# Optimization experiments

Hardware: AMD Instinct MI355X
Metric: run time of the kernel (lower is better)

## Reference

```python
import jax, jax.numpy as jnp
import numpy as np

GL16 = [5, 3, 3, 3, 3, 3, 5, 5, 5, 11, 3, 3, 3, 3, 3, 12]  # sum 73
GL7 = [5, 9, 9, 25, 9, 9, 12]  # sum 78
BN_EPS = 1e-5
LRELU_SLOPE = 0.01


def setup_inputs() -> dict:
    key = jax.random.key(0)
    ks = jax.random.split(key, 32)
    B = 65536
    u = lambda k, shp, s: jax.random.uniform(k, shp, minval=-s, maxval=s)
    inp = {}
    inp['x'] = jax.random.normal(ks[0], (B, 310), dtype=jnp.float32)
    # learned adjacency (convert_dis_m(get_ini_dis_m(), 9) placeholder)
    inp['adj'] = jax.random.normal(ks[1], (62, 62), dtype=jnp.float32) * 0.1
    s5 = 1.0 / np.sqrt(5.0)
    inp['lgcn_w'] = u(ks[2], (5, 5), s5)
    inp['lgcn_b'] = u(ks[3], (5,), s5)
    # ChannelAttentionMPL (frequency, C=5) conv1d k=1 weights [out,in]
    inp['ca1_w1'] = jax.random.normal(ks[4], (32, 5)) * 0.3
    inp['ca1_w2'] = jax.random.normal(ks[5], (5, 32)) * 0.1
    # ChannelAttentionMPL (channel, C=62)
    inp['ca2_w1'] = jax.random.normal(ks[6], (32, 62)) * 0.1
    inp['ca2_w2'] = jax.random.normal(ks[7], (62, 32)) * 0.1
    # MesoLayer weights [5,10]
    inp['meso1_w'] = u(ks[8], (5, 10), 1.0 / np.sqrt(78.0))
    inp['meso2_w'] = u(ks[9], (5, 10), 1.0 / np.sqrt(78.0))
    # graphpool.feature_trans index maps (channel gathers into 62 channels)
    inp['idx16'] = jax.random.randint(ks[10], (73,), 0, 62, dtype=jnp.int32)
    inp['idx7'] = jax.random.randint(ks[11], (78,), 0, 62, dtype=jnp.int32)
    # MLP head 735->256->128->64 with eval-mode BatchNorm params
    def lin(ka, kb, fin, fout):
        s = 1.0 / np.sqrt(fin)
        return u(ka, (fin, fout), s), u(kb, (fout,), s)
    inp['w1'], inp['b1'] = lin(ks[12], ks[13], 735, 256)
    inp['w2'], inp['b2'] = lin(ks[14], ks[15], 256, 128)
    inp['w3'], inp['b3'] = lin(ks[16], ks[17], 128, 64)
    for i, (nm, d) in enumerate([('1', 256), ('2', 128), ('3', 64)]):
        inp['g' + nm] = 1.0 + 0.1 * jax.random.normal(ks[18 + 3 * i], (d,))
        inp['be' + nm] = 0.1 * jax.random.normal(ks[19 + 3 * i], (d,))
        inp['m' + nm] = 0.05 * jax.random.normal(ks[20 + 3 * i], (d,))
        inp['v' + nm] = jnp.ones((d,), dtype=jnp.float32)
    return inp


def channel_attention(x, w1, w2):
    # x: [B, C, L]; SE-style attention with avg+max pooling over L
    avg = jnp.mean(x, axis=2)            # [B, C]
    mx = jnp.max(x, axis=2)              # [B, C]
    def mlp(z):
        return jax.nn.relu(z @ w1.T) @ w2.T   # [B, C]
    att = jax.nn.sigmoid(mlp(avg) + mlp(mx))[:, :, None]  # [B, C, 1]
    return x + att * x, att


def meso(feat, idx, weight, graph_list):
    # feat: [B, 62, 5]; gather channels then per-subgraph attention pooling
    f = feat[:, idx]                     # [B, L, 5]
    outs = []
    h = 0
    for n in graph_list:                 # fixed small structural loop
        sub = jax.lax.dynamic_slice_in_dim(f, h, n, axis=1)  # [B, n, 5]
        fw = jnp.einsum('bjg,gh->bjh', sub, weight)          # [B, n, 10]
        # sum_i (fw @ fw^T)[b,j,i] == fw[b,j,:] . sum_i fw[b,i,:]
        scores = jnp.einsum('bjh,bh->bj', fw, jnp.sum(fw, axis=1))  # [B, n]
        att = jax.nn.softmax(scores, axis=1)
        outs.append(jnp.einsum('bj,bjg->bg', att, sub))      # [B, 5]
        h += n
    return jnp.stack(outs, axis=1)       # [B, S, 5]


def _forward(x, adj, lgcn_w, lgcn_b, ca1_w1, ca1_w2, ca2_w1, ca2_w2,
             meso1_w, meso2_w, idx16, idx7,
             w1, b1, g1, be1, m1, v1,
             w2, b2, g2, be2, m2, v2,
             w3, b3, g3, be3, m3, v3):
    B = x.shape[0]
    h = x.reshape(B, 5, 62).transpose(0, 2, 1)                   # [B, 62, 5]
    wf = jnp.einsum('bij,jd->bid', h, lgcn_w)
    h = jnp.einsum('ij,bjd->bid', adj, wf) + lgcn_b              # LocalLayer
    residual = h
    hx = h.transpose(0, 2, 1)                                    # [B, 5, 62]
    x_flat = hx.reshape(B, -1)                                   # [B, 310]
    out, att1 = channel_attention(hx, ca1_w1, ca1_w2)            # [B, 5, 62]
    out, att2 = channel_attention(out.transpose(0, 2, 1), ca2_w1, ca2_w2)  # [B,62,5]
    x1 = meso(residual, idx16, meso1_w, GL16).transpose(0, 2, 1).reshape(B, -1)  # [B, 80]
    x3 = meso(residual, idx7, meso2_w, GL7).transpose(0, 2, 1).reshape(B, -1)    # [B, 35]
    out_flat = out.transpose(0, 2, 1).reshape(B, -1)             # [B, 310]
    cat = jnp.concatenate([x_flat, out_flat, x1, x3], axis=1)    # [B, 735]

    def block(z, w, b, g, be, m, v):
        y = z @ w + b
        y = (y - m) / jnp.sqrt(v + BN_EPS) * g + be              # eval BN
        return jnp.where(y > 0, y, LRELU_SLOPE * y)              # LeakyReLU

    y = block(cat, w1, b1, g1, be1, m1, v1)
    y = block(y, w2, b2, g2, be2, m2, v2)
    y = block(y, w3, b3, g3, be3, m3, v3)
    return y, att1, att2


def reference(x, adj, lgcn_w, lgcn_b, ca1_w1, ca1_w2, ca2_w1, ca2_w2,
              meso1_w, meso2_w, idx16, idx7,
              w1, b1, w2, b2, w3, b3,
              g1, be1, m1, v1, g2, be2, m2, v2, g3, be3, m3, v3):
    return _forward(x, adj, lgcn_w, lgcn_b, ca1_w1, ca1_w2, ca2_w1, ca2_w2,
                    meso1_w, meso2_w, idx16, idx7,
                    w1, b1, g1, be1, m1, v1,
                    w2, b2, g2, be2, m2, v2,
                    w3, b3, g3, be3, m3, v3)
```

## Files before the change

### kernel.cpp

```cpp
#include <hip/hip_runtime.h>
#include <math.h>

#define BN_EPS 1e-5f
#define SLOPE 0.01f

typedef _Float16 f16;
typedef _Float16 f16x8 __attribute__((ext_vector_type(8)));
typedef float f32x4 __attribute__((ext_vector_type(4)));

__device__ __constant__ int c_g16_st[16] = {0,5,8,11,14,17,20,25,30,35,46,49,52,55,58,61};
__device__ __constant__ int c_g16_n[16]  = {5,3,3,3,3,3,5,5,5,11,3,3,3,3,3,12};
__device__ __constant__ int c_g7_st[7]   = {0,5,14,23,48,57,66};
__device__ __constant__ int c_g7_n[7]    = {5,9,9,25,9,9,12};

__device__ __forceinline__ float lrelu(float y) { return y > 0.f ? y : SLOPE * y; }

template<int T, int G, int BASE>
__device__ void meso_part(const int* __restrict__ st_arr, const int* __restrict__ n_arr,
                          int lane, long b, const float* h, const int* __restrict__ idxa,
                          const float* mw, float* fwbuf, float* scbuf,
                          f16* __restrict__ catb)
{
  const int team = lane / T, slot = lane - team * T;
  int st = 0, n = 0;
  if (team < G) { st = st_arr[team]; n = n_arr[team]; }
  float sp[10] = {0,0,0,0,0,0,0,0,0,0};
  if (team < G) {
    for (int j = slot; j < n; j += T) {
      int ri = idxa[st + j];
      float sv[5];
      #pragma unroll
      for (int g = 0; g < 5; ++g) sv[g] = h[ri*8 + g];
      #pragma unroll
      for (int t = 0; t < 10; ++t) {
        float f = sv[0]*mw[t] + sv[1]*mw[10+t] + sv[2]*mw[20+t] + sv[3]*mw[30+t] + sv[4]*mw[40+t];
        fwbuf[(st+j)*10 + t] = f;
        sp[t] += f;
      }
    }
  }
  #pragma unroll
  for (int off = 1; off < T; off <<= 1) {
    #pragma unroll
    for (int t = 0; t < 10; ++t) sp[t] += __shfl_xor(sp[t], off);
  }
  __syncthreads();
  if (team < G) {
    for (int j = slot; j < n; j += T) {
      float sc = 0.f;
      #pragma unroll
      for (int t = 0; t < 10; ++t) sc += fwbuf[(st+j)*10 + t] * sp[t];
      scbuf[st + j] = sc;
    }
  }
  __syncthreads();
  float po[5] = {0,0,0,0,0};
  if (team < G) {
    float mx = -1e30f;
    for (int jj = 0; jj < n; ++jj) mx = fmaxf(mx, scbuf[st + jj]);
    float sum = 0.f;
    for (int jj = 0; jj < n; ++jj) sum += expf(scbuf[st + jj] - mx);
    float inv = 1.f / sum;
    for (int j = slot; j < n; j += T) {
      float a = expf(scbuf[st + j] - mx) * inv;
      int ri = idxa[st + j];
      #pragma unroll
      for (int g = 0; g < 5; ++g) po[g] += a * h[ri*8 + g];
    }
  }
  #pragma unroll
  for (int off = 1; off < T; off <<= 1) {
    #pragma unroll
    for (int g = 0; g < 5; ++g) po[g] += __shfl_xor(po[g], off);
  }
  if (team < G && slot == 0) {
    #pragma unroll
    for (int g = 0; g < 5; ++g) catb[b*736 + BASE + g*G + team] = (f16)po[g];
  }
}

__global__ void wcvt_kernel(const float* __restrict__ w1, const float* __restrict__ w2,
                            const float* __restrict__ w3,
                            const float* __restrict__ adj, const float* __restrict__ lgcn_w,
                            f16* __restrict__ w1T, f16* __restrict__ w2T, f16* __restrict__ w3T,
                            f16* __restrict__ Mp)
{
  int i = blockIdx.x * 256 + threadIdx.x;
  if (i < 256*736) {
    int n = i / 736, k = i - n*736;
    w1T[i] = (f16)(k < 735 ? w1[k*256 + n] : 0.f);
    return;
  }
  int j = i - 256*736;
  if (j < 128*256) {
    int n = j >> 8, k = j & 255;
    w2T[j] = (f16)w2[k*128 + n];
    return;
  }
  int q = j - 128*256;
  if (q < 64*128) {
    int n = q >> 7, k = q & 127;
    w3T[q] = (f16)w3[k*64 + n];
    return;
  }
  int m = q - 64*128;
  if (m < 320*320) {
    int col = m / 320, k = m - col*320;
    float v = 0.f;
    if (col < 310 && k < 310) {
      int d = col / 62, ii = col - d*62;
      int g = k / 62,  jj = k - g*62;
      v = adj[ii*62 + jj] * lgcn_w[g*5 + d];
    }
    Mp[m] = (f16)v;
  }
}

__global__ __launch_bounds__(256) void gemm_h(
    const float* __restrict__ x, const f16* __restrict__ Mp,
    const float* __restrict__ lgcn_b, f16* __restrict__ catb)
{
  __shared__ __align__(16) f16 a_lds[64*320];

  const int tid = threadIdx.x;
  const int wv = tid >> 6;
  const int lane = tid & 63;
  const int ln = lane & 15;
  const int kg = lane >> 4;
  const long b0 = (long)blockIdx.x * 64;

  const f16* mp[5];
  #pragma unroll
  for (int nc = 0; nc < 5; ++nc)
    mp[nc] = Mp + (size_t)(wv*80 + nc*16 + ln)*320 + kg*8;
  f16x8 bF[5], bN[5];
  #pragma unroll
  for (int nc = 0; nc < 5; ++nc) bF[nc] = *(const f16x8*)(mp[nc]);

  for (int rr = 0; rr < 16; ++rr) {
    int row = wv*16 + rr;
    if (lane < 8) {
      int c = 38 + (lane >> 2);
      *(unsigned*)((char*)a_lds + row*640 + ((c ^ (row & 7)) << 4) + (lane & 3)*4) = 0u;
    }
    const float* xr = x + (b0 + row)*310;
    for (int f = lane; f < 155; f += 64) {
      float2 v = *(const float2*)(xr + 2*f);
      int k = 2*f;
      int c = k >> 3;
      f16 h0 = (f16)v.x, h1 = (f16)v.y;
      unsigned u = (unsigned)*(unsigned short*)&h0 | ((unsigned)*(unsigned short*)&h1 << 16);
      *(unsigned*)((char*)a_lds + row*640 + ((c ^ (row & 7)) << 4) + (k & 7)*2) = u;
    }
  }
  __syncthreads();

  f32x4 zero = {0.f, 0.f, 0.f, 0.f};
  f32x4 acc[4][5];
  #pragma unroll
  for (int mr = 0; mr < 4; ++mr)
    #pragma unroll
    for (int nc = 0; nc < 5; ++nc) acc[mr][nc] = zero;

  for (int s = 0; s < 10; ++s) {
    if (s < 9) {
      #pragma unroll
      for (int nc = 0; nc < 5; ++nc) bN[nc] = *(const f16x8*)(mp[nc] + (s + 1)*32);
    }
    #pragma unroll
    for (int mr = 0; mr < 4; ++mr) {
      int r = mr*16 + ln;
      int c = s*4 + kg;
      f16x8 af = *(const f16x8*)((const char*)a_lds + r*640 + ((c ^ (r & 7)) << 4));
      #pragma unroll
      for (int nc = 0; nc < 5; ++nc)
        acc[mr][nc] = __builtin_amdgcn_mfma_f32_16x16x32_f16(af, bF[nc], acc[mr][nc], 0, 0, 0);
    }
    #pragma unroll
    for (int nc = 0; nc < 5; ++nc) bF[nc] = bN[nc];
  }

  __syncthreads();
  #pragma unroll
  for (int nc = 0; nc < 5; ++nc) {
    int n = wv*80 + nc*16 + ln;
    float bias = (n < 310) ? lgcn_b[n / 62] : 0.f;
    int c = n >> 3;
    #pragma unroll
    for (int mr = 0; mr < 4; ++mr) {
      #pragma unroll
      for (int ri = 0; ri < 4; ++ri) {
        int r = mr*16 + kg*4 + ri;
        f16 val = (f16)(acc[mr][nc][ri] + bias);
        *(f16*)((char*)a_lds + r*640 + ((c ^ (r & 7)) << 4) + (n & 7)*2) = val;
      }
    }
  }
  __syncthreads();
  for (int rr = 0; rr < 16; ++rr) {
    int row = wv*16 + rr;
    if (lane < 39) {
      int c = lane;
      f16x8 v = *(const f16x8*)((const char*)a_lds + row*640 + ((c ^ (row & 7)) << 4));
      *(f16x8*)(catb + (b0 + row)*736 + c*8) = v;
    }
  }
}

__global__ __launch_bounds__(256) void front2(
    const float* __restrict__ ca1_w1, const float* __restrict__ ca1_w2,
    const float* __restrict__ ca2_w1, const float* __restrict__ ca2_w2,
    const float* __restrict__ meso1_w, const float* __restrict__ meso2_w,
    const int* __restrict__ idx16, const int* __restrict__ idx7,
    f16* __restrict__ catb, float* __restrict__ outp, int B)
{
  __shared__ __align__(16) float h_s[4][496];
  __shared__ __align__(16) float fw_s[4][800];
  __shared__ float sc_s[4][80];
  __shared__ float t_s[4][64];
  __shared__ float small_s[4][16];
  __shared__ float v62_s[4][192];
  __shared__ float mw_s[100];

  const int tid = threadIdx.x;
  const int w = tid >> 6;
  const int lane = tid & 63;
  const long b = (long)blockIdx.x * 4 + w;

  if (tid < 50) mw_s[tid] = meso1_w[tid];
  else if (tid < 100) mw_s[tid] = meso2_w[tid - 50];

  for (int p = lane; p < 310; p += 64) {
    float v = (float)catb[b*736 + p];
    int d = p / 62, i = p - d*62;
    h_s[w][i*8 + d] = v;
  }
  __syncthreads();

  {
    int d = lane >> 3, q = lane & 7;
    float s = 0.f, m = -1e30f;
    if (d < 5) {
      #pragma unroll
      for (int e = 0; e < 8; ++e) {
        int i = q*8 + e;
        if (i < 62) { float v = h_s[w][i*8 + d]; s += v; m = fmaxf(m, v); }
      }
    }
    #pragma unroll
    for (int off = 1; off < 8; off <<= 1) {
      s += __shfl_xor(s, off);
      m = fmaxf(m, __shfl_xor(m, off));
    }
    if (d < 5 && q == 0) {
      small_s[w][d] = s * (1.f/62.f);
      small_s[w][5 + d] = m;
    }
  }
  __syncthreads();
  if (lane < 32) {
    float ta = 0.f, tm = 0.f;
    #pragma unroll
    for (int d = 0; d < 5; ++d) {
      float wv = ca1_w1[lane*5 + d];
      ta += small_s[w][d] * wv;
      tm += small_s[w][5 + d] * wv;
    }
    t_s[w][lane] = fmaxf(ta, 0.f);
    t_s[w][32 + lane] = fmaxf(tm, 0.f);
  }
  __syncthreads();
  if (lane < 5) {
    float sa = 0.f, sm = 0.f;
    for (int o = 0; o < 32; ++o) {
      float wv = ca1_w2[lane*32 + o];
      sa += t_s[w][o] * wv; sm += t_s[w][32 + o] * wv;
    }
    float a = 1.f / (1.f + expf(-(sa + sm)));
    small_s[w][10 + lane] = a;
    outp[(long)B*64 + b*5 + lane] = a;
  }
  __syncthreads();
  if (lane < 62) {
    float s = 0.f, m = -1e30f;
    #pragma unroll
    for (int d = 0; d < 5; ++d) {
      float v = h_s[w][lane*8 + d] * (1.f + small_s[w][10 + d]);
      s += v; m = fmaxf(m, v);
    }
    v62_s[w][lane] = s * (1.f/5.f);
    v62_s[w][64 + lane] = m;
  }
  __syncthreads();
  {
    int half = lane >> 5;
    int o = lane & 31;
    const float* src = &v62_s[w][half*64];
    float t = 0.f;
    for (int i = 0; i < 62; ++i) t += src[i] * ca2_w1[o*62 + i];
    t_s[w][half*32 + o] = fmaxf(t, 0.f);
  }
  __syncthreads();
  if (lane < 62) {
    float sa = 0.f, sm = 0.f;
    for (int o = 0; o < 32; ++o) {
      float wv = ca2_w2[lane*32 + o];
      sa += t_s[w][o] * wv; sm += t_s[w][32 + o] * wv;
    }
    float a = 1.f / (1.f + expf(-(sa + sm)));
    v62_s[w][128 + lane] = a;
    outp[(long)B*69 + b*62 + lane] = a;
  }
  __syncthreads();
  for (int p = lane; p < 310; p += 64) {
    int d = p / 62, i = p - d*62;
    catb[b*736 + 310 + p] = (f16)(h_s[w][i*8 + d] * (1.f + small_s[w][10 + d]) * (1.f + v62_s[w][128 + i]));
  }
  if (lane == 0) catb[b*736 + 735] = (f16)0.f;
  __syncthreads();
  meso_part<4,16,620>(c_g16_st, c_g16_n, lane, b, h_s[w], idx16, mw_s, fw_s[w], sc_s[w], catb);
  __syncthreads();
  meso_part<8,7,700>(c_g7_st, c_g7_n, lane, b, h_s[w], idx7, mw_s + 50, fw_s[w], sc_s[w], catb);
}

__global__ __launch_bounds__(256) void mlp_mfma(
    const f16* __restrict__ cat,
    const f16* __restrict__ w1T, const f16* __restrict__ w2T, const f16* __restrict__ w3T,
    const float* __restrict__ b1, const float* __restrict__ g1, const float* __restrict__ be1,
    const float* __restrict__ m1, const float* __restrict__ v1,
    const float* __restrict__ b2, const float* __restrict__ g2, const float* __restrict__ be2,
    const float* __restrict__ m2, const float* __restrict__ v2,
    const float* __restrict__ b3, const float* __restrict__ g3, const float* __restrict__ be3,
    const float* __restrict__ m3, const float* __restrict__ v3,
    float* __restrict__ outp)
{
  __shared__ __align__(16) f16 a_lds[64*32];
  __shared__ __align__(16) f16 y1s[64*256];
  __shared__ __align__(16) f16 y2s[64*128];

  const int tid = threadIdx.x;
  const int wv = tid >> 6;
  const int lane = tid & 63;
  const int ln = lane & 15;
  const int kg = lane >> 4;
  const long b0 = (long)blockIdx.x * 64;

  f32x4 zero = {0.f, 0.f, 0.f, 0.f};
  f32x4 acc1[4][4];
  #pragma unroll
  for (int i = 0; i < 4; ++i)
    #pragma unroll
    for (int j = 0; j < 4; ++j) acc1[i][j] = zero;

  const int sr  = tid >> 2;
  const int scs = tid & 3;
  const int sdst = sr*64 + ((scs ^ ((sr >> 1) & 3)) << 4);
  const f16* aSrc = cat + (b0 + sr)*736 + scs*8;

  int aoff[4];
  #pragma unroll
  for (int mr = 0; mr < 4; ++mr) {
    int r = mr*16 + ln;
    aoff[mr] = r*64 + ((kg ^ ((r >> 1) & 3)) << 4);
  }

  const f16* w1p[4];
  #pragma unroll
  for (int nc = 0; nc < 4; ++nc)
    w1p[nc] = w1T + (size_t)(wv*64 + nc*16 + ln)*736 + kg*8;

  f16x8 bF[4], bN[4];
  #pragma unroll
  for (int nc = 0; nc < 4; ++nc) bF[nc] = *(const f16x8*)(w1p[nc]);
  f16x8 aReg = *(const f16x8*)(aSrc);
  f16x8 aRegN;

  for (int s = 0; s < 23; ++s) {
    __syncthreads();
    *(f16x8*)((char*)a_lds + sdst) = aReg;
    __syncthreads();
    if (s < 22) {
      aRegN = *(const f16x8*)(aSrc + (s + 1)*32);
      #pragma unroll
      for (int nc = 0; nc < 4; ++nc) bN[nc] = *(const f16x8*)(w1p[nc] + (s + 1)*32);
    }
    #pragma unroll
    for (int mr = 0; mr < 4; ++mr) {
      f16x8 af = *(const f16x8*)((const char*)a_lds + aoff[mr]);
      #pragma unroll
      for (int nc = 0; nc < 4; ++nc)
        acc1[mr][nc] = __builtin_amdgcn_mfma_f32_16x16x32_f16(af, bF[nc], acc1[mr][nc], 0, 0, 0);
    }
    aReg = aRegN;
    #pragma unroll
    for (int nc = 0; nc < 4; ++nc) bF[nc] = bN[nc];
  }

  #pragma unroll
  for (int nc = 0; nc < 4; ++nc) {
    int n = wv*64 + nc*16 + ln;
    float sc = g1[n] * rsqrtf(v1[n] + BN_EPS);
    float bm = b1[n] - m1[n];
    float bo = be1[n];
    int c = n >> 3;
    #pragma unroll
    for (int mr = 0; mr < 4; ++mr) {
      #pragma unroll
      for (int ri = 0; ri < 4; ++ri) {
        int r = mr*16 + kg*4 + ri;
        float y = lrelu((acc1[mr][nc][ri] + bm)*sc + bo);
        int off = r*512 + ((c ^ (r & 7)) << 4) + ((n & 7) << 1);
        *(f16*)((char*)y1s + off) = (f16)y;
      }
    }
  }
  __syncthreads();

  f32x4 acc2[4][2];
  #pragma unroll
  for (int i = 0; i < 4; ++i) { acc2[i][0] = zero; acc2[i][1] = zero; }
  const f16* w2p[2];
  #pragma unroll
  for (int nc = 0; nc < 2; ++nc)
    w2p[nc] = w2T + (size_t)(wv*32 + nc*16 + ln)*256 + kg*8;

  #pragma unroll
  for (int s2 = 0; s2 < 8; ++s2) {
    f16x8 b2f[2];
    #pragma unroll
    for (int nc = 0; nc < 2; ++nc) b2f[nc] = *(const f16x8*)(w2p[nc] + s2*32);
    #pragma unroll
    for (int mr = 0; mr < 4; ++mr) {
      int r = mr*16 + ln;
      int c = s2*4 + kg;
      f16x8 af = *(const f16x8*)((const char*)y1s + r*512 + ((c ^ (r & 7)) << 4));
      #pragma unroll
      for (int nc = 0; nc < 2; ++nc)
        acc2[mr][nc] = __builtin_amdgcn_mfma_f32_16x16x32_f16(af, b2f[nc], acc2[mr][nc], 0, 0, 0);
    }
  }
  #pragma unroll
  for (int nc = 0; nc < 2; ++nc) {
    int n = wv*32 + nc*16 + ln;
    float sc = g2[n] * rsqrtf(v2[n] + BN_EPS);
    float bm = b2[n] - m2[n];
    float bo = be2[n];
    int c = n >> 3;
    #pragma unroll
    for (int mr = 0; mr < 4; ++mr) {
      #pragma unroll
      for (int ri = 0; ri < 4; ++ri) {
        int r = mr*16 + kg*4 + ri;
        float y = lrelu((acc2[mr][nc][ri] + bm)*sc + bo);
        int off = r*256 + ((c ^ (r & 7)) << 4) + ((n & 7) << 1);
        *(f16*)((char*)y2s + off) = (f16)y;
      }
    }
  }
  __syncthreads();

  f32x4 acc3[4];
  #pragma unroll
  for (int i = 0; i < 4; ++i) acc3[i] = zero;
  const f16* w3p = w3T + (size_t)(wv*16 + ln)*128 + kg*8;

  #pragma unroll
  for (int s3 = 0; s3 < 4; ++s3) {
    f16x8 bf = *(const f16x8*)(w3p + s3*32);
    #pragma unroll
    for (int mr = 0; mr < 4; ++mr) {
      int r = mr*16 + ln;
      int c = s3*4 + kg;
      f16x8 af = *(const f16x8*)((const char*)y2s + r*256 + ((c ^ (r & 7)) << 4));
      acc3[mr] = __builtin_amdgcn_mfma_f32_16x16x32_f16(af, bf, acc3[mr], 0, 0, 0);
    }
  }
  {
    int n = wv*16 + ln;
    float sc = g3[n] * rsqrtf(v3[n] + BN_EPS);
    float bm = b3[n] - m3[n];
    float bo = be3[n];
    #pragma unroll
    for (int mr = 0; mr < 4; ++mr) {
      #pragma unroll
      for (int ri = 0; ri < 4; ++ri) {
        int r = mr*16 + kg*4 + ri;
        float y = lrelu((acc3[mr][ri] + bm)*sc + bo);
        outp[(size_t)(b0 + r)*64 + n] = y;
      }
    }
  }
}

extern "C" void kernel_launch(void* const* d_in, const int* in_sizes, int n_in,
                              void* d_out, int out_size, void* d_ws, size_t ws_size,
                              hipStream_t stream) {
  const float* x       = (const float*)d_in[0];
  const float* adj     = (const float*)d_in[1];
  const float* lgcn_w  = (const float*)d_in[2];
  const float* lgcn_b  = (const float*)d_in[3];
  const float* ca1_w1  = (const float*)d_in[4];
  const float* ca1_w2  = (const float*)d_in[5];
  const float* ca2_w1  = (const float*)d_in[6];
  const float* ca2_w2  = (const float*)d_in[7];
  const float* meso1_w = (const float*)d_in[8];
  const float* meso2_w = (const float*)d_in[9];
  const int*   idx16   = (const int*)d_in[10];
  const int*   idx7    = (const int*)d_in[11];
  const float* w1 = (const float*)d_in[12];
  const float* b1 = (const float*)d_in[13];
  const float* w2 = (const float*)d_in[14];
  const float* b2 = (const float*)d_in[15];
  const float* w3 = (const float*)d_in[16];
  const float* b3 = (const float*)d_in[17];
  const float* g1 = (const float*)d_in[18];
  const float* be1= (const float*)d_in[19];
  const float* m1 = (const float*)d_in[20];
  const float* v1 = (const float*)d_in[21];
  const float* g2 = (const float*)d_in[22];
  const float* be2= (const float*)d_in[23];
  const float* m2 = (const float*)d_in[24];
  const float* v2 = (const float*)d_in[25];
  const float* g3 = (const float*)d_in[26];
  const float* be3= (const float*)d_in[27];
  const float* m3 = (const float*)d_in[28];
  const float* v3 = (const float*)d_in[29];

  const int B = in_sizes[0] / 310;

  const size_t catBytes = (size_t)B * 736 * sizeof(f16);
  char* wsc = (char*)d_ws;
  f16* catb = (f16*)wsc;
  f16* w1T  = (f16*)(wsc + catBytes);
  f16* w2T  = (f16*)(wsc + catBytes + 256*736*sizeof(f16));
  f16* w3T  = (f16*)(wsc + catBytes + (256*736 + 128*256)*sizeof(f16));
  f16* Mp   = (f16*)(wsc + catBytes + (256*736 + 128*256 + 64*128)*sizeof(f16));
  const size_t need = catBytes + (256*736 + 128*256 + 64*128 + 320*320)*sizeof(f16);
  if (ws_size < need) return;

  const int prepElems = 256*736 + 128*256 + 64*128 + 320*320;
  wcvt_kernel<<<(prepElems + 255)/256, 256, 0, stream>>>(w1, w2, w3, adj, lgcn_w,
                                                         w1T, w2T, w3T, Mp);
  gemm_h<<<B/64, 256, 0, stream>>>(x, Mp, lgcn_b, catb);
  front2<<<B/4, 256, 0, stream>>>(ca1_w1, ca1_w2, ca2_w1, ca2_w2, meso1_w, meso2_w,
                                  idx16, idx7, catb, (float*)d_out, B);
  mlp_mfma<<<B/64, 256, 0, stream>>>(catb, w1T, w2T, w3T,
                                     b1, g1, be1, m1, v1,
                                     b2, g2, be2, m2, v2,
                                     b3, g3, be3, m3, v3, (float*)d_out);
}
```

Before: 640.7 us.

## Restructure front2 with register-resident meso attention and wave-local LDS syncs

Replaces block-wide __syncthreads with wave-local lgkmcnt waits, since each wave handles its own batch row. Stages the small attention weights and index maps in LDS, with the ca2 weights transposed to f16. The meso softmax keeps per-row features in registers and computes the scores algebraically as sv·(W·sp), so the fw buffer is gone. Also pads the h layout to stride 9, uses fast exp, and sets a 5-block occupancy hint. The risk is that relying on lgkmcnt waits instead of barriers for cross-lane LDS visibility may be unsafe if the compiler reorders accesses. The f16 weights also slightly reduce precision.

```diff
diff --git a/kernel.cpp b/kernel.cpp
--- a/kernel.cpp
+++ b/kernel.cpp
@@ -3,6 +3,8 @@
 
 #define BN_EPS 1e-5f
 #define SLOPE 0.01f
+
+#define WSYNC() asm volatile("s_waitcnt lgkmcnt(0)" ::: "memory")
 
 typedef _Float16 f16;
 typedef _Float16 f16x8 __attribute__((ext_vector_type(8)));
@@ -15,64 +17,79 @@
 
 __device__ __forceinline__ float lrelu(float y) { return y > 0.f ? y : SLOPE * y; }
 
-template<int T, int G, int BASE>
-__device__ void meso_part(const int* __restrict__ st_arr, const int* __restrict__ n_arr,
-                          int lane, long b, const float* h, const int* __restrict__ idxa,
-                          const float* mw, float* fwbuf, float* scbuf,
-                          f16* __restrict__ catb)
+template<int T, int G, int R, int BASE>
+__device__ void meso_reg(const int* __restrict__ st_arr, const int* __restrict__ n_arr,
+                         int lane, long b, const float* h, const int* idx_s,
+                         const float* mw, float* scb, f16* __restrict__ catb)
 {
   const int team = lane / T, slot = lane - team * T;
   int st = 0, n = 0;
   if (team < G) { st = st_arr[team]; n = n_arr[team]; }
+
+  float sv[R][5];
+  bool act[R];
   float sp[10] = {0,0,0,0,0,0,0,0,0,0};
-  if (team < G) {
-    for (int j = slot; j < n; j += T) {
-      int ri = idxa[st + j];
-      float sv[5];
-      #pragma unroll
-      for (int g = 0; g < 5; ++g) sv[g] = h[ri*8 + g];
-      #pragma unroll
-      for (int t = 0; t < 10; ++t) {
-        float f = sv[0]*mw[t] + sv[1]*mw[10+t] + sv[2]*mw[20+t] + sv[3]*mw[30+t] + sv[4]*mw[40+t];
-        fwbuf[(st+j)*10 + t] = f;
-        sp[t] += f;
-      }
-    }
-  }
-  #pragma unroll
-  for (int off = 1; off < T; off <<= 1) {
+  #pragma unroll
+  for (int rr = 0; rr < R; ++rr) {
+    int j = slot + rr*T;
+    act[rr] = (team < G) && (j < n);
+    #pragma unroll
+    for (int g = 0; g < 5; ++g) sv[rr][g] = 0.f;
+    if (act[rr]) {
+      int ri = idx_s[st + j];
+      #pragma unroll
+      for (int g = 0; g < 5; ++g) sv[rr][g] = h[ri*9 + g];
+      #pragma unroll
+      for (int t = 0; t < 10; ++t)
+        sp[t] += sv[rr][0]*mw[t] + sv[rr][1]*mw[10+t] + sv[rr][2]*mw[20+t]
+               + sv[rr][3]*mw[30+t] + sv[rr][4]*mw[40+t];
+    }
+  }
+  #pragma unroll
+  for (int off = 1; off < T; off <<= 1)
     #pragma unroll
     for (int t = 0; t < 10; ++t) sp[t] += __shfl_xor(sp[t], off);
-  }
-  __syncthreads();
-  if (team < G) {
-    for (int j = slot; j < n; j += T) {
-      float sc = 0.f;
-      #pragma unroll
-      for (int t = 0; t < 10; ++t) sc += fwbuf[(st+j)*10 + t] * sp[t];
-      scbuf[st + j] = sc;
-    }
-  }
-  __syncthreads();
+
+  float qs[5];
+  #pragma unroll
+  for (int g = 0; g < 5; ++g) {
+    float q = 0.f;
+    #pragma unroll
+    for (int t = 0; t < 10; ++t) q += mw[g*10 + t] * sp[t];
+    qs[g] = q;
+  }
+  float sc_own[R];
+  #pragma unroll
+  for (int rr = 0; rr < R; ++rr) {
+    float sc = sv[rr][0]*qs[0] + sv[rr][1]*qs[1] + sv[rr][2]*qs[2]
+             + sv[rr][3]*qs[3] + sv[rr][4]*qs[4];
+    sc_own[rr] = sc;
+    if (act[rr]) scb[st + slot + rr*T] = sc;
+  }
+  WSYNC();
+  float mx = -1e30f;
+  for (int jj = 0; jj < n; ++jj) mx = fmaxf(mx, scb[st + jj]);
+  float e_own[R];
+  #pragma unroll
+  for (int rr = 0; rr < R; ++rr) e_own[rr] = __expf(sc_own[rr] - mx);
+  WSYNC();
+  #pragma unroll
+  for (int rr = 0; rr < R; ++rr) if (act[rr]) scb[st + slot + rr*T] = e_own[rr];
+  WSYNC();
+  float sum = 0.f;
+  for (int jj = 0; jj < n; ++jj) sum += scb[st + jj];
+  float inv = 1.f / sum;
   float po[5] = {0,0,0,0,0};
-  if (team < G) {
-    float mx = -1e30f;
-    for (int jj = 0; jj < n; ++jj) mx = fmaxf(mx, scbuf[st + jj]);
-    float sum = 0.f;
-    for (int jj = 0; jj < n; ++jj) sum += expf(scbuf[st + jj] - mx);
-    float inv = 1.f / sum;
-    for (int j = slot; j < n; j += T) {
-      float a = expf(scbuf[st + j] - mx) * inv;
-      int ri = idxa[st + j];
-      #pragma unroll
-      for (int g = 0; g < 5; ++g) po[g] += a * h[ri*8 + g];
-    }
-  }
-  #pragma unroll
-  for (int off = 1; off < T; off <<= 1) {
+  #pragma unroll
+  for (int rr = 0; rr < R; ++rr) if (act[rr]) {
+    float a = e_own[rr] * inv;
+    #pragma unroll
+    for (int g = 0; g < 5; ++g) po[g] += a * sv[rr][g];
+  }
+  #pragma unroll
+  for (int off = 1; off < T; off <<= 1)
     #pragma unroll
     for (int g = 0; g < 5; ++g) po[g] += __shfl_xor(po[g], off);
-  }
   if (team < G && slot == 0) {
     #pragma unroll
     for (int g = 0; g < 5; ++g) catb[b*736 + BASE + g*G + team] = (f16)po[g];
@@ -207,35 +224,53 @@
   }
 }
 
-__global__ __launch_bounds__(256) void front2(
+__global__ __launch_bounds__(256, 5) void front2(
     const float* __restrict__ ca1_w1, const float* __restrict__ ca1_w2,
     const float* __restrict__ ca2_w1, const float* __restrict__ ca2_w2,
     const float* __restrict__ meso1_w, const float* __restrict__ meso2_w,
     const int* __restrict__ idx16, const int* __restrict__ idx7,
     f16* __restrict__ catb, float* __restrict__ outp, int B)
 {
-  __shared__ __align__(16) float h_s[4][496];
-  __shared__ __align__(16) float fw_s[4][800];
+  __shared__ float h_s[4][560];
   __shared__ float sc_s[4][80];
   __shared__ float t_s[4][64];
   __shared__ float small_s[4][16];
-  __shared__ float v62_s[4][192];
+  __shared__ float v62_s[4][128];
   __shared__ float mw_s[100];
+  __shared__ float c1a_s[160];
+  __shared__ float c1b_s[160];
+  __shared__ f16  w1c_s[62*32];
+  __shared__ f16  w2c_s[32*64];
+  __shared__ int  idx16_s[73];
+  __shared__ int  idx7_s[78];
 
   const int tid = threadIdx.x;
   const int w = tid >> 6;
   const int lane = tid & 63;
   const long b = (long)blockIdx.x * 4 + w;
 
-  if (tid < 50) mw_s[tid] = meso1_w[tid];
-  else if (tid < 100) mw_s[tid] = meso2_w[tid - 50];
-
-  for (int p = lane; p < 310; p += 64) {
-    float v = (float)catb[b*736 + p];
-    int d = p / 62, i = p - d*62;
-    h_s[w][i*8 + d] = v;
+  if (tid < 100) mw_s[tid] = (tid < 50) ? meso1_w[tid] : meso2_w[tid - 50];
+  if (tid < 160) { c1a_s[tid] = ca1_w1[tid]; c1b_s[tid] = ca1_w2[tid]; }
+  if (tid < 73) idx16_s[tid] = idx16[tid];
+  if (tid < 78) idx7_s[tid] = idx7[tid];
+  for (int t = tid; t < 62*32; t += 256) {
+    int i = t >> 5, o = t & 31;
+    w1c_s[t] = (f16)ca2_w1[o*62 + i];
+  }
+  for (int t = tid; t < 62*32; t += 256) {
+    int o = t / 62, i = t - o*62;
+    w2c_s[o*64 + i] = (f16)ca2_w2[i*32 + o];
   }
   __syncthreads();
+
+  float hv[5] = {0,0,0,0,0};
+  if (lane < 62) {
+    #pragma unroll
+    for (int d = 0; d < 5; ++d) hv[d] = (float)catb[b*736 + d*62 + lane];
+    #pragma unroll
+    for (int d = 0; d < 5; ++d) h_s[w][lane*9 + d] = hv[d];
+  }
+  WSYNC();
 
   {
     int d = lane >> 3, q = lane & 7;
@@ -244,7 +279,7 @@
       #pragma unroll
       for (int e = 0; e < 8; ++e) {
         int i = q*8 + e;
-        if (i < 62) { float v = h_s[w][i*8 + d]; s += v; m = fmaxf(m, v); }
+        if (i < 62) { float v = h_s[w][i*9 + d]; s += v; m = fmaxf(m, v); }
       }
     }
     #pragma unroll
@@ -257,70 +292,73 @@
       small_s[w][5 + d] = m;
     }
   }
-  __syncthreads();
+  WSYNC();
   if (lane < 32) {
     float ta = 0.f, tm = 0.f;
     #pragma unroll
     for (int d = 0; d < 5; ++d) {
-      float wv = ca1_w1[lane*5 + d];
+      float wv = c1a_s[lane*5 + d];
       ta += small_s[w][d] * wv;
       tm += small_s[w][5 + d] * wv;
     }
     t_s[w][lane] = fmaxf(ta, 0.f);
     t_s[w][32 + lane] = fmaxf(tm, 0.f);
   }
-  __syncthreads();
+  WSYNC();
   if (lane < 5) {
     float sa = 0.f, sm = 0.f;
+    #pragma unroll 4
     for (int o = 0; o < 32; ++o) {
-      float wv = ca1_w2[lane*32 + o];
+      float wv = c1b_s[lane*32 + o];
       sa += t_s[w][o] * wv; sm += t_s[w][32 + o] * wv;
     }
-    float a = 1.f / (1.f + expf(-(sa + sm)));
+    float a = 1.f / (1.f + __expf(-(sa + sm)));
     small_s[w][10 + lane] = a;
     outp[(long)B*64 + b*5 + lane] = a;
   }
-  __syncthreads();
+  WSYNC();
+  float a1f[5];
+  #pragma unroll
+  for (int d = 0; d < 5; ++d) a1f[d] = 1.f + small_s[w][10 + d];
   if (lane < 62) {
     float s = 0.f, m = -1e30f;
     #pragma unroll
     for (int d = 0; d < 5; ++d) {
-      float v = h_s[w][lane*8 + d] * (1.f + small_s[w][10 + d]);
+      float v = hv[d] * a1f[d];
       s += v; m = fmaxf(m, v);
     }
     v62_s[w][lane] = s * (1.f/5.f);
     v62_s[w][64 + lane] = m;
   }
-  __syncthreads();
+  WSYNC();
   {
     int half = lane >> 5;
     int o = lane & 31;
     const float* src = &v62_s[w][half*64];
     float t = 0.f;
-    for (int i = 0; i < 62; ++i) t += src[i] * ca2_w1[o*62 + i];
+    #pragma unroll 2
+    for (int i = 0; i < 62; ++i) t += src[i] * (float)w1c_s[i*32 + o];
     t_s[w][half*32 + o] = fmaxf(t, 0.f);
   }
-  __syncthreads();
+  WSYNC();
   if (lane < 62) {
     float sa = 0.f, sm = 0.f;
+    #pragma unroll 4
     for (int o = 0; o < 32; ++o) {
-      float wv = ca2_w2[lane*32 + o];
+      float wv = (float)w2c_s[o*64 + lane];
       sa += t_s[w][o] * wv; sm += t_s[w][32 + o] * wv;
     }
-    float a = 1.f / (1.f + expf(-(sa + sm)));
-    v62_s[w][128 + lane] = a;
-    outp[(long)B*69 + b*62 + lane] = a;
-  }
-  __syncthreads();
-  for (int p = lane; p < 310; p += 64) {
-    int d = p / 62, i = p - d*62;
-    catb[b*736 + 310 + p] = (f16)(h_s[w][i*8 + d] * (1.f + small_s[w][10 + d]) * (1.f + v62_s[w][128 + i]));
+    float a2 = 1.f / (1.f + __expf(-(sa + sm)));
+    outp[(long)B*69 + b*62 + lane] = a2;
+    float f2 = 1.f + a2;
+    #pragma unroll
+    for (int d = 0; d < 5; ++d)
+      catb[b*736 + 310 + d*62 + lane] = (f16)(hv[d] * a1f[d] * f2);
   }
   if (lane == 0) catb[b*736 + 735] = (f16)0.f;
-  __syncthreads();
-  meso_part<4,16,620>(c_g16_st, c_g16_n, lane, b, h_s[w], idx16, mw_s, fw_s[w], sc_s[w], catb);
-  __syncthreads();
-  meso_part<8,7,700>(c_g7_st, c_g7_n, lane, b, h_s[w], idx7, mw_s + 50, fw_s[w], sc_s[w], catb);
+
+  meso_reg<4,16,3,620>(c_g16_st, c_g16_n, lane, b, h_s[w], idx16_s, mw_s, sc_s[w], catb);
+  meso_reg<8,7,4,700>(c_g7_st, c_g7_n, lane, b, h_s[w], idx7_s, mw_s + 50, sc_s[w], catb);
 }
 
 __global__ __launch_bounds__(256) void mlp_mfma(
```

New measurement: 575.9 us. -10.1%, faster.
